# Kernel tuning notes

Hardware: AMD Instinct MI355X
Metric: run time of the kernel (lower is better)

## Reference

```python
import jax, jax.numpy as jnp
import numpy as np

ALPHA = 0.2
NEG = -9e15
EPS = 1e-5


def _gat(h, adj, W, a, out_features):
    # h: [B,N,Fin], adj: [B,N,N], W: [Fin,Fout], a: [2*Fout,1]
    Wh = jnp.matmul(h, W)                      # [B,N,Fout]
    Wh1 = jnp.matmul(Wh, a[:out_features])     # [B,N,1]
    Wh2 = jnp.matmul(Wh, a[out_features:])     # [B,N,1]
    e = Wh1 + jnp.swapaxes(Wh2, 1, 2)          # [B,N,N]
    e = jax.nn.leaky_relu(e, negative_slope=ALPHA)
    scores = jnp.where(adj > 0, e, NEG)
    att = jax.nn.softmax(scores, axis=1)       # NOTE: dim=1 as in source
    return jnp.matmul(att, Wh)                 # [B,N,Fout]


def _layernorm(x, g, b):
    mu = jnp.mean(x, axis=-1, keepdims=True)
    var = jnp.var(x, axis=-1, keepdims=True)
    return (x - mu) * jax.lax.rsqrt(var + EPS) * g + b


def setup_inputs() -> dict:
    key = jax.random.key(0)
    ks = jax.random.split(key, 8)
    B, N, F, H = 2, 4096, 256, 1024
    x = jax.random.normal(ks[0], (B, N, F), dtype=jnp.float32)
    adj = jax.random.randint(ks[1], (B, N, N), 0, 2, dtype=jnp.int32)
    def xavier(k, shape):
        fan_in, fan_out = shape[0], shape[1]
        lim = np.sqrt(6.0 / (fan_in + fan_out))
        return jax.random.uniform(k, shape, jnp.float32, -lim, lim)
    return {
        "x": x,
        "adj": adj,
        "W1": xavier(ks[2], (F, F)),
        "a1": xavier(ks[3], (2 * F, 1)),
        "W2": xavier(ks[4], (F, F)),
        "a2": xavier(ks[5], (2 * F, 1)),
        "w_ff1": xavier(ks[6], (F, H)) ,
        "b_ff1": jnp.zeros((H,), jnp.float32),
        "w_ff2": xavier(ks[7], (H, F)),
        "b_ff2": jnp.zeros((F,), jnp.float32),
        "g_ln1": jnp.ones((F,), jnp.float32),
        "b_ln1": jnp.zeros((F,), jnp.float32),
        "g_ln2": jnp.ones((F,), jnp.float32),
        "b_ln2": jnp.zeros((F,), jnp.float32),
    }


def reference(x, adj, W1, a1, W2, a2, w_ff1, b_ff1, w_ff2, b_ff2,
              g_ln1, b_ln1, g_ln2, b_ln2):
    Fout = W1.shape[1]
    residual = x
    # dropout is a no-op in eval mode
    h = _gat(x, adj, W1, a1, Fout)          # single head -> cat is identity
    h = _gat(h, adj, W2, a2, W2.shape[1])
    h = _layernorm(residual + h, g_ln1, b_ln1)
    residual2 = h
    ff = jnp.matmul(jax.nn.relu(jnp.matmul(h, w_ff1) + b_ff1), w_ff2) + b_ff2
    return _layernorm(residual2 + ff, g_ln2, b_ln2)
```

## Files before the change

kernel.cpp:

```cpp
#include <hip/hip_runtime.h>
#include <math.h>

#define ALPHA 0.2f
#define NEGV  -9e15f
#define EPSV  1e-5f

constexpr int B_ = 2, N_ = 4096, F_ = 256, H_ = 1024;
constexpr int SPLIT_ = 16;
constexpr int SPLITJ_ = 4;

typedef __attribute__((ext_vector_type(4))) float f32x4;
typedef __attribute__((ext_vector_type(8))) short s16x8;

__device__ __forceinline__ unsigned short f2bf(float f) {
    unsigned u = __builtin_bit_cast(unsigned, f);
    u += 0x7fffu + ((u >> 16) & 1u);
    return (unsigned short)(u >> 16);
}

__global__ __launch_bounds__(256) void gemm_bf16_kernel(
    const float* __restrict__ A, const unsigned short* __restrict__ Wt,
    const float* __restrict__ bias, float* __restrict__ C,
    int M, int Nc, int K, int relu)
{
    __shared__ unsigned short As[64 * 72];
    __shared__ unsigned short Bs[64 * 72];
    const int t = threadIdx.x;
    const int w = t >> 6, l = t & 63;
    const int quad = l >> 4, l15 = l & 15;
    const int iw = (w & 1) * 32, fw = (w >> 1) * 32;
    const int row0 = blockIdx.y * 64, col0 = blockIdx.x * 64;

    const int sr = t >> 2;
    const int sk = (t & 3) * 16;

    f32x4 acc[2][2];
    #pragma unroll
    for (int a = 0; a < 2; ++a)
        #pragma unroll
        for (int c = 0; c < 2; ++c) acc[a][c] = (f32x4)(0.f);

    for (int k0 = 0; k0 < K; k0 += 64) {
        {
            const float* ap = &A[(size_t)(row0 + sr) * K + k0 + sk];
            #pragma unroll
            for (int u4 = 0; u4 < 4; ++u4) {
                const float4 v = *(const float4*)&ap[u4 * 4];
                ushort4 o;
                o.x = f2bf(v.x); o.y = f2bf(v.y); o.z = f2bf(v.z); o.w = f2bf(v.w);
                *(ushort4*)&As[sr * 72 + sk + u4 * 4] = o;
            }
        }
        {
            const unsigned short* bp = &Wt[(size_t)(col0 + sr) * K + k0 + sk];
            *(s16x8*)&Bs[sr * 72 + sk]     = *(const s16x8*)bp;
            *(s16x8*)&Bs[sr * 72 + sk + 8] = *(const s16x8*)(bp + 8);
        }
        __syncthreads();
        #pragma unroll
        for (int ks = 0; ks < 64; ks += 32) {
            s16x8 af[2], bf[2];
            #pragma unroll
            for (int it = 0; it < 2; ++it)
                af[it] = *(const s16x8*)&As[(iw + it * 16 + l15) * 72 + ks + quad * 8];
            #pragma unroll
            for (int ft = 0; ft < 2; ++ft)
                bf[ft] = *(const s16x8*)&Bs[(fw + ft * 16 + l15) * 72 + ks + quad * 8];
            #pragma unroll
            for (int it = 0; it < 2; ++it)
                #pragma unroll
                for (int ft = 0; ft < 2; ++ft)
                    acc[it][ft] = __builtin_amdgcn_mfma_f32_16x16x32_bf16(
                        af[it], bf[ft], acc[it][ft], 0, 0, 0);
        }
        __syncthreads();
    }

    #pragma unroll
    for (int ft = 0; ft < 2; ++ft) {
        const int col = col0 + fw + ft * 16 + l15;
        const float bv = bias ? bias[col] : 0.f;
        #pragma unroll
        for (int it = 0; it < 2; ++it) {
            #pragma unroll
            for (int rr = 0; rr < 4; ++rr) {
                const int row = row0 + iw + it * 16 + quad * 4 + rr;
                float v = acc[it][ft][rr] + bv;
                if (relu) v = fmaxf(v, 0.f);
                C[(size_t)row * Nc + col] = v;
            }
        }
    }
}

__global__ __launch_bounds__(256) void wh12_kernel(
    const float* __restrict__ Wh, const float* __restrict__ a,
    float* __restrict__ Wh1, float* __restrict__ Wh2)
{
    const int wid = threadIdx.x >> 6, lane = threadIdx.x & 63;
    const int row = blockIdx.x * 4 + wid;
    const float4 w  = *(const float4*)&Wh[(size_t)row * F_ + lane * 4];
    const float4 u1 = *(const float4*)&a[lane * 4];
    const float4 u2 = *(const float4*)&a[F_ + lane * 4];
    float s1 = w.x * u1.x + w.y * u1.y + w.z * u1.z + w.w * u1.w;
    float s2 = w.x * u2.x + w.y * u2.y + w.z * u2.z + w.w * u2.w;
    #pragma unroll
    for (int off = 32; off > 0; off >>= 1) {
        s1 += __shfl_down(s1, off);
        s2 += __shfl_down(s2, off);
    }
    if (lane == 0) { Wh1[row] = s1; Wh2[row] = s2; }
}

__global__ __launch_bounds__(256) void maskpack_kernel(
    const int* __restrict__ adj, unsigned long long* __restrict__ mask)
{
    const int t = threadIdx.x;
    const int w = t >> 6, l = t & 63;
    const int wid = blockIdx.x * 4 + w;
    const int nw = gridDim.x * 4;
    const int nchunks = (B_ * N_ * N_) / 256;
    for (int c = wid; c < nchunks; c += nw) {
        const size_t base = (size_t)c * 256;
        #pragma unroll
        for (int r = 0; r < 4; ++r) {
            const int v = adj[base + r * 64 + l];
            const unsigned long long bm = __ballot(v > 0);
            if (l == 0) mask[base / 64 + r] = bm;
        }
    }
}

__global__ __launch_bounds__(256) void colstats3_kernel(
    const unsigned long long* __restrict__ mask,
    const float* __restrict__ Wh1, const float* __restrict__ Wh2,
    float* __restrict__ pM, float* __restrict__ pS)
{
    const int t = threadIdx.x;
    const int j = blockIdx.x * 256 + t;
    const int sp = blockIdx.y;
    const int b = blockIdx.z;
    const int i0 = sp * (N_ / SPLIT_);
    const int w = t >> 6;
    const int jbit = t & 63;
    const float w2 = Wh2[b * N_ + j];
    const unsigned long long* __restrict__ mbase =
        mask + ((size_t)b * N_ + i0) * (N_ / 64) + blockIdx.x * 4 + w;
    const float* __restrict__ w1p = Wh1 + b * N_ + i0;

    float m = -3.4e38f, s = 0.f;
    for (int c = 0; c < N_ / SPLIT_; c += 8) {
        float x[8];
        #pragma unroll
        for (int u = 0; u < 8; ++u) {
            const unsigned long long mw = mbase[(size_t)(c + u) * (N_ / 64)];
            const float e0 = w1p[c + u] + w2;
            const float e = fmaxf(e0, ALPHA * e0);
            x[u] = ((mw >> jbit) & 1ull) ? e : NEGV;
        }
        float cm = fmaxf(fmaxf(fmaxf(x[0], x[1]), fmaxf(x[2], x[3])),
                         fmaxf(fmaxf(x[4], x[5]), fmaxf(x[6], x[7])));
        const float nm = fmaxf(m, cm);
        float cs = 0.f;
        #pragma unroll
        for (int u = 0; u < 8; ++u) cs += __expf(x[u] - nm);
        s = s * __expf(m - nm) + cs;
        m = nm;
    }
    pM[((size_t)b * SPLIT_ + sp) * N_ + j] = m;
    pS[((size_t)b * SPLIT_ + sp) * N_ + j] = s;
}

__global__ __launch_bounds__(256) void colfin_kernel(
    const float* __restrict__ pM, const float* __restrict__ pS,
    float* __restrict__ Mcol, float* __restrict__ Sinv)
{
    const int j = blockIdx.x * 256 + threadIdx.x;
    const int b = blockIdx.y;
    float m = -3.4e38f;
    #pragma unroll
    for (int s = 0; s < SPLIT_; ++s)
        m = fmaxf(m, pM[((size_t)b * SPLIT_ + s) * N_ + j]);
    float sum = 0.f;
    #pragma unroll
    for (int s = 0; s < SPLIT_; ++s)
        sum += pS[((size_t)b * SPLIT_ + s) * N_ + j] *
               __expf(pM[((size_t)b * SPLIT_ + s) * N_ + j] - m);
    Mcol[b * N_ + j] = m;
    Sinv[b * N_ + j] = 1.0f / sum;
}

__global__ __launch_bounds__(256) void transp_kernel(
    const float* __restrict__ src, unsigned short* __restrict__ dst, int R, int Cc)
{
    __shared__ float T[64][65];
    const int t = threadIdx.x;
    const int r0 = blockIdx.x * 64, c0 = blockIdx.y * 64;
    const size_t boff = (size_t)blockIdx.z * R * Cc;
    #pragma unroll
    for (int s = 0; s < 4; ++s) {
        const int rr = s * 16 + (t >> 4);
        const int cq = t & 15;
        const float4 v = *(const float4*)&src[boff + (size_t)(r0 + rr) * Cc + c0 + cq * 4];
        T[rr][cq * 4 + 0] = v.x; T[rr][cq * 4 + 1] = v.y;
        T[rr][cq * 4 + 2] = v.z; T[rr][cq * 4 + 3] = v.w;
    }
    __syncthreads();
    #pragma unroll
    for (int s = 0; s < 4; ++s) {
        const int cr = s * 16 + (t >> 4);
        const int rq = t & 15;
        ushort4 o;
        o.x = f2bf(T[rq * 4 + 0][cr]);
        o.y = f2bf(T[rq * 4 + 1][cr]);
        o.z = f2bf(T[rq * 4 + 2][cr]);
        o.w = f2bf(T[rq * 4 + 3][cr]);
        *(ushort4*)&dst[boff + (size_t)(c0 + cr) * R + r0 + rq * 4] = o;
    }
}

__global__ __launch_bounds__(256) void att_mfma2_kernel(
    const unsigned short* __restrict__ mask16, const unsigned short* __restrict__ Wht,
    const float* __restrict__ Wh1, const float* __restrict__ Wh2,
    const float* __restrict__ Mcol, const float* __restrict__ Sinv,
    float* __restrict__ part)
{
    __shared__ unsigned short Bs[256 * 72];
    __shared__ unsigned short Ps[64 * 72];

    const int t = threadIdx.x;
    const int w = t >> 6, l = t & 63;
    const int quad = l >> 4, l15 = l & 15;
    const int b = blockIdx.z;
    const int i0 = blockIdx.x * 64;
    const int sp = blockIdx.y;
    const int jbase = sp * (N_ / SPLITJ_);

    const int pi = t >> 2;
    const int pj4 = t & 3;
    const float w1i = Wh1[b * N_ + i0 + pi];
    const unsigned short* __restrict__ mrow =
        mask16 + ((size_t)b * N_ + i0 + pi) * (N_ / 16);

    f32x4 acc[4][4];
    #pragma unroll
    for (int it = 0; it < 4; ++it)
        #pragma unroll
        for (int ft = 0; ft < 4; ++ft) acc[it][ft] = (f32x4)(0.f);

    const unsigned short* __restrict__ WhtB = Wht + (size_t)b * F_ * N_;
    const float* __restrict__ w2B = Wh2 + b * N_;
    const float* __restrict__ mB  = Mcol + b * N_;
    const float* __restrict__ sB  = Sinv + b * N_;

    for (int itr = 0; itr < (N_ / SPLITJ_) / 64; ++itr) {
        const int jb = jbase + itr * 64;
        #pragma unroll
        for (int s = 0; s < 8; ++s) {
            const int idx = t + s * 256;
            const int f = idx >> 3, prt = idx & 7;
            *(s16x8*)&Bs[f * 72 + prt * 8] =
                *(const s16x8*)&WhtB[(size_t)f * N_ + jb + prt * 8];
        }
        {
            const unsigned mb = mrow[jb / 16 + pj4];
            #pragma unroll
            for (int u4 = 0; u4 < 4; ++u4) {
                const int jo = pj4 * 16 + u4 * 4;
                const float4 w2v = *(const float4*)&w2B[jb + jo];
                const float4 mv  = *(const float4*)&mB[jb + jo];
                const float4 sv  = *(const float4*)&sB[jb + jo];
                ushort4 o;
                unsigned short* op = &o.x;
                #pragma unroll
                for (int u = 0; u < 4; ++u) {
                    const float xw = w1i + (&w2v.x)[u];
                    const float e = fmaxf(xw, ALPHA * xw);
                    const float x2 = ((mb >> (u4 * 4 + u)) & 1u) ? e : NEGV;
                    op[u] = f2bf(__expf(x2 - (&mv.x)[u]) * (&sv.x)[u]);
                }
                *(ushort4*)&Ps[pi * 72 + jo] = o;
            }
        }
        __syncthreads();
        #pragma unroll
        for (int ks = 0; ks < 64; ks += 32) {
            s16x8 af[4];
            #pragma unroll
            for (int it = 0; it < 4; ++it)
                af[it] = *(const s16x8*)&Ps[(it * 16 + l15) * 72 + ks + quad * 8];
            #pragma unroll
            for (int ft = 0; ft < 4; ++ft) {
                const s16x8 bf =
                    *(const s16x8*)&Bs[(w * 64 + ft * 16 + l15) * 72 + ks + quad * 8];
                #pragma unroll
                for (int it = 0; it < 4; ++it)
                    acc[it][ft] = __builtin_amdgcn_mfma_f32_16x16x32_bf16(
                        af[it], bf, acc[it][ft], 0, 0, 0);
            }
        }
        __syncthreads();
    }

    float* __restrict__ pout = part + ((size_t)sp * B_ + b) * N_ * F_;
    #pragma unroll
    for (int it = 0; it < 4; ++it)
        #pragma unroll
        for (int ft = 0; ft < 4; ++ft) {
            const int col = w * 64 + ft * 16 + l15;
            #pragma unroll
            for (int rr = 0; rr < 4; ++rr) {
                const int row = i0 + it * 16 + quad * 4 + rr;
                pout[(size_t)row * F_ + col] = acc[it][ft][rr];
            }
        }
}

__global__ __launch_bounds__(256) void reduce4_kernel(
    const float* __restrict__ p, float* __restrict__ out)
{
    const size_t i = ((size_t)blockIdx.x * 256 + threadIdx.x) * 4;
    const size_t S = (size_t)B_ * N_ * F_;
    const float4 a = *(const float4*)&p[i];
    const float4 b = *(const float4*)&p[i + S];
    const float4 c = *(const float4*)&p[i + 2 * S];
    const float4 d = *(const float4*)&p[i + 3 * S];
    float4 o;
    o.x = a.x + b.x + c.x + d.x;
    o.y = a.y + b.y + c.y + d.y;
    o.z = a.z + b.z + c.z + d.z;
    o.w = a.w + b.w + c.w + d.w;
    *(float4*)&out[i] = o;
}

__global__ __launch_bounds__(256) void addln_kernel(
    const float* __restrict__ X, const float* __restrict__ Y,
    const float* __restrict__ g, const float* __restrict__ bta,
    float* __restrict__ out)
{
    const int row = blockIdx.x;
    const int t = threadIdx.x;
    const size_t idx = (size_t)row * F_ + t;
    const float v = X[idx] + Y[idx];
    float s1 = v, s2 = v * v;
    #pragma unroll
    for (int off = 32; off > 0; off >>= 1) {
        s1 += __shfl_down(s1, off);
        s2 += __shfl_down(s2, off);
    }
    __shared__ float r1[4], r2[4];
    __shared__ float mu_s, rs_s;
    const int wid = t >> 6, lane = t & 63;
    if (lane == 0) { r1[wid] = s1; r2[wid] = s2; }
    __syncthreads();
    if (t == 0) {
        const float a = r1[0] + r1[1] + r1[2] + r1[3];
        const float q = r2[0] + r2[1] + r2[2] + r2[3];
        const float mu = a * (1.f / F_);
        const float var = q * (1.f / F_) - mu * mu;
        mu_s = mu;
        rs_s = rsqrtf(var + EPSV);
    }
    __syncthreads();
    out[idx] = (v - mu_s) * rs_s * g[t] + bta[t];
}

extern "C" void kernel_launch(void* const* d_in, const int* in_sizes, int n_in,
                              void* d_out, int out_size, void* d_ws, size_t ws_size,
                              hipStream_t stream)
{
    const float* x     = (const float*)d_in[0];
    const int*   adj   = (const int*)d_in[1];
    const float* W1    = (const float*)d_in[2];
    const float* a1    = (const float*)d_in[3];
    const float* W2    = (const float*)d_in[4];
    const float* a2    = (const float*)d_in[5];
    const float* w_ff1 = (const float*)d_in[6];
    const float* b_ff1 = (const float*)d_in[7];
    const float* w_ff2 = (const float*)d_in[8];
    const float* b_ff2 = (const float*)d_in[9];
    const float* g_ln1 = (const float*)d_in[10];
    const float* b_ln1 = (const float*)d_in[11];
    const float* g_ln2 = (const float*)d_in[12];
    const float* b_ln2 = (const float*)d_in[13];
    float* out = (float*)d_out;

    const int Rtot = B_ * N_;
    float* ws = (float*)d_ws;
    float* Wh_buf = ws;
    float* ln1    = ws;
    float* g1out  = ws + 2097152;
    float* part   = ws + 4194304;
    float* mid    = ws + 4194304;
    unsigned short* Wht = (unsigned short*)(ws + 12582912);
    unsigned short* Wt  = (unsigned short*)(ws + 12582912);
    unsigned long long* mask = (unsigned long long*)(ws + 13631488);
    unsigned short* mask16 = (unsigned short*)mask;
    float* Wh1v = ws + 14680064;
    float* Wh2v = Wh1v + 8192;
    float* Mcol = Wh2v + 8192;
    float* Sinv = Mcol + 8192;
    float* pM   = Sinv + 8192;
    float* pS   = pM + (size_t)B_ * SPLIT_ * N_;

    const dim3 statsG(N_ / 256, SPLIT_, B_);
    const dim3 finG(N_ / 256, B_);
    const dim3 attG(N_ / 64, SPLITJ_, B_);
    const dim3 trWhG(N_ / 64, F_ / 64, B_);

    maskpack_kernel<<<2048, 256, 0, stream>>>(adj, mask);

    transp_kernel<<<dim3(4, 4, 1), 256, 0, stream>>>(W1, Wt, 256, 256);
    gemm_bf16_kernel<<<dim3(F_ / 64, Rtot / 64), 256, 0, stream>>>(x, Wt, nullptr, Wh_buf, Rtot, F_, F_, 0);
    wh12_kernel<<<Rtot / 4, 256, 0, stream>>>(Wh_buf, a1, Wh1v, Wh2v);
    colstats3_kernel<<<statsG, 256, 0, stream>>>(mask, Wh1v, Wh2v, pM, pS);
    colfin_kernel<<<finG, 256, 0, stream>>>(pM, pS, Mcol, Sinv);
    transp_kernel<<<trWhG, 256, 0, stream>>>(Wh_buf, Wht, N_, F_);
    att_mfma2_kernel<<<attG, 256, 0, stream>>>(mask16, Wht, Wh1v, Wh2v, Mcol, Sinv, part);
    reduce4_kernel<<<2048, 256, 0, stream>>>(part, g1out);

    transp_kernel<<<dim3(4, 4, 1), 256, 0, stream>>>(W2, Wt, 256, 256);
    gemm_bf16_kernel<<<dim3(F_ / 64, Rtot / 64), 256, 0, stream>>>(g1out, Wt, nullptr, Wh_buf, Rtot, F_, F_, 0);
    wh12_kernel<<<Rtot / 4, 256, 0, stream>>>(Wh_buf, a2, Wh1v, Wh2v);
    colstats3_kernel<<<statsG, 256, 0, stream>>>(mask, Wh1v, Wh2v, pM, pS);
    colfin_kernel<<<finG, 256, 0, stream>>>(pM, pS, Mcol, Sinv);
    transp_kernel<<<trWhG, 256, 0, stream>>>(Wh_buf, Wht, N_, F_);
    att_mfma2_kernel<<<attG, 256, 0, stream>>>(mask16, Wht, Wh1v, Wh2v, Mcol, Sinv, part);
    reduce4_kernel<<<2048, 256, 0, stream>>>(part, g1out);

    addln_kernel<<<Rtot, 256, 0, stream>>>(x, g1out, g_ln1, b_ln1, ln1);

    transp_kernel<<<dim3(4, 16, 1), 256, 0, stream>>>(w_ff1, Wt, 256, 1024);
    gemm_bf16_kernel<<<dim3(H_ / 64, Rtot / 64), 256, 0, stream>>>(ln1, Wt, b_ff1, mid, Rtot, H_, F_, 1);
    transp_kernel<<<dim3(16, 4, 1), 256, 0, stream>>>(w_ff2, Wt, 1024, 256);
    gemm_bf16_kernel<<<dim3(F_ / 64, Rtot / 64), 256, 0, stream>>>(mid, Wt, b_ff2, out, Rtot, F_, H_, 0);

    addln_kernel<<<Rtot, 256, 0, stream>>>(ln1, out, g_ln2, b_ln2, out);
}
```

Before: 464.6 us.

## Fuse mask packing into column stats, GEMM transposed output, and log-sum-exp softmax

Several changes at once. The adjacency bitmask is now packed inside the first column-stats pass, which drops the separate maskpack pass over the int32 adj. The Wh GEMM writes a transposed bf16 copy of its output directly, removing the standalone transpose kernels. The softmax normalizer is folded into one log-sum-exp value, so the attention kernel loads one fewer vector, caches Wh2 and Mo in shared memory, and prefetches the next Wht tile into registers. The FFN intermediate is also stored in bf16 to halve its traffic, at some precision cost and with a larger workspace footprint.

```diff
diff --git a/kernel.cpp b/kernel.cpp
--- a/kernel.cpp
+++ b/kernel.cpp
@@ -18,10 +18,11 @@
     return (unsigned short)(u >> 16);
 }
 
-__global__ __launch_bounds__(256) void gemm_bf16_kernel(
-    const float* __restrict__ A, const unsigned short* __restrict__ Wt,
-    const float* __restrict__ bias, float* __restrict__ C,
-    int M, int Nc, int K, int relu)
+__global__ __launch_bounds__(256) void gemm2_kernel(
+    const void* __restrict__ Ap, const unsigned short* __restrict__ Wt,
+    const float* __restrict__ bias, void* __restrict__ Cp,
+    unsigned short* __restrict__ Tout,
+    int M, int Nc, int K, int relu, int a_bf16, int c_bf16)
 {
     __shared__ unsigned short As[64 * 72];
     __shared__ unsigned short Bs[64 * 72];
@@ -41,8 +42,13 @@
         for (int c = 0; c < 2; ++c) acc[a][c] = (f32x4)(0.f);
 
     for (int k0 = 0; k0 < K; k0 += 64) {
-        {
-            const float* ap = &A[(size_t)(row0 + sr) * K + k0 + sk];
+        if (a_bf16) {
+            const unsigned short* ap =
+                (const unsigned short*)Ap + (size_t)(row0 + sr) * K + k0 + sk;
+            *(s16x8*)&As[sr * 72 + sk]     = *(const s16x8*)ap;
+            *(s16x8*)&As[sr * 72 + sk + 8] = *(const s16x8*)(ap + 8);
+        } else {
+            const float* ap = (const float*)Ap + (size_t)(row0 + sr) * K + k0 + sk;
             #pragma unroll
             for (int u4 = 0; u4 < 4; ++u4) {
                 const float4 v = *(const float4*)&ap[u4 * 4];
@@ -82,12 +88,33 @@
         const float bv = bias ? bias[col] : 0.f;
         #pragma unroll
         for (int it = 0; it < 2; ++it) {
-            #pragma unroll
-            for (int rr = 0; rr < 4; ++rr) {
-                const int row = row0 + iw + it * 16 + quad * 4 + rr;
-                float v = acc[it][ft][rr] + bv;
-                if (relu) v = fmaxf(v, 0.f);
-                C[(size_t)row * Nc + col] = v;
+            float v0 = acc[it][ft][0] + bv, v1 = acc[it][ft][1] + bv;
+            float v2 = acc[it][ft][2] + bv, v3 = acc[it][ft][3] + bv;
+            if (relu) {
+                v0 = fmaxf(v0, 0.f); v1 = fmaxf(v1, 0.f);
+                v2 = fmaxf(v2, 0.f); v3 = fmaxf(v3, 0.f);
+            }
+            const int rbase = row0 + iw + it * 16 + quad * 4;
+            if (c_bf16) {
+                unsigned short* Cs = (unsigned short*)Cp;
+                Cs[(size_t)(rbase + 0) * Nc + col] = f2bf(v0);
+                Cs[(size_t)(rbase + 1) * Nc + col] = f2bf(v1);
+                Cs[(size_t)(rbase + 2) * Nc + col] = f2bf(v2);
+                Cs[(size_t)(rbase + 3) * Nc + col] = f2bf(v3);
+            } else {
+                float* Cf = (float*)Cp;
+                Cf[(size_t)(rbase + 0) * Nc + col] = v0;
+                Cf[(size_t)(rbase + 1) * Nc + col] = v1;
+                Cf[(size_t)(rbase + 2) * Nc + col] = v2;
+                Cf[(size_t)(rbase + 3) * Nc + col] = v3;
+            }
+            if (Tout) {
+                const int bb = row0 >> 12;
+                const int ibase = (row0 & (N_ - 1)) + iw + it * 16 + quad * 4;
+                ushort4 o;
+                o.x = f2bf(acc[it][ft][0]); o.y = f2bf(acc[it][ft][1]);
+                o.z = f2bf(acc[it][ft][2]); o.w = f2bf(acc[it][ft][3]);
+                *(ushort4*)&Tout[((size_t)bb * F_ + col) * N_ + ibase] = o;
             }
         }
     }
@@ -112,23 +139,48 @@
     if (lane == 0) { Wh1[row] = s1; Wh2[row] = s2; }
 }
 
-__global__ __launch_bounds__(256) void maskpack_kernel(
-    const int* __restrict__ adj, unsigned long long* __restrict__ mask)
+__global__ __launch_bounds__(256) void colstats_adj_kernel(
+    const int* __restrict__ adj, unsigned long long* __restrict__ maskOut,
+    const float* __restrict__ Wh1, const float* __restrict__ Wh2,
+    float* __restrict__ pM, float* __restrict__ pS)
 {
     const int t = threadIdx.x;
+    const int j = blockIdx.x * 256 + t;
+    const int sp = blockIdx.y;
+    const int b = blockIdx.z;
+    const int i0 = sp * (N_ / SPLIT_);
     const int w = t >> 6, l = t & 63;
-    const int wid = blockIdx.x * 4 + w;
-    const int nw = gridDim.x * 4;
-    const int nchunks = (B_ * N_ * N_) / 256;
-    for (int c = wid; c < nchunks; c += nw) {
-        const size_t base = (size_t)c * 256;
-        #pragma unroll
-        for (int r = 0; r < 4; ++r) {
-            const int v = adj[base + r * 64 + l];
-            const unsigned long long bm = __ballot(v > 0);
-            if (l == 0) mask[base / 64 + r] = bm;
-        }
-    }
+    const float w2 = Wh2[b * N_ + j];
+    const float* __restrict__ w1p = Wh1 + b * N_ + i0;
+    const int* __restrict__ ap = adj + ((size_t)b * N_ + i0) * N_ + j;
+
+    float m = -3.4e38f, s = 0.f;
+    for (int c = 0; c < N_ / SPLIT_; c += 8) {
+        int v[8];
+        #pragma unroll
+        for (int u = 0; u < 8; ++u) v[u] = ap[(size_t)(c + u) * N_];
+        float x[8];
+        #pragma unroll
+        for (int u = 0; u < 8; ++u) {
+            const bool act = v[u] > 0;
+            const unsigned long long bm = __ballot(act);
+            if (l == 0)
+                maskOut[((size_t)b * N_ + i0 + c + u) * (N_ / 64) + blockIdx.x * 4 + w] = bm;
+            const float e0 = w1p[c + u] + w2;
+            const float e = fmaxf(e0, ALPHA * e0);
+            x[u] = act ? e : NEGV;
+        }
+        const float cm = fmaxf(fmaxf(fmaxf(x[0], x[1]), fmaxf(x[2], x[3])),
+                               fmaxf(fmaxf(x[4], x[5]), fmaxf(x[6], x[7])));
+        const float nm = fmaxf(m, cm);
+        float cs = 0.f;
+        #pragma unroll
+        for (int u = 0; u < 8; ++u) cs += __expf(x[u] - nm);
+        s = s * __expf(m - nm) + cs;
+        m = nm;
+    }
+    pM[((size_t)b * SPLIT_ + sp) * N_ + j] = m;
+    pS[((size_t)b * SPLIT_ + sp) * N_ + j] = s;
 }
 
 __global__ __launch_bounds__(256) void colstats3_kernel(
@@ -158,8 +210,8 @@
             const float e = fmaxf(e0, ALPHA * e0);
             x[u] = ((mw >> jbit) & 1ull) ? e : NEGV;
         }
-        float cm = fmaxf(fmaxf(fmaxf(x[0], x[1]), fmaxf(x[2], x[3])),
-                         fmaxf(fmaxf(x[4], x[5]), fmaxf(x[6], x[7])));
+        const float cm = fmaxf(fmaxf(fmaxf(x[0], x[1]), fmaxf(x[2], x[3])),
+                               fmaxf(fmaxf(x[4], x[5]), fmaxf(x[6], x[7])));
         const float nm = fmaxf(m, cm);
         float cs = 0.f;
         #pragma unroll
@@ -171,9 +223,9 @@
     pS[((size_t)b * SPLIT_ + sp) * N_ + j] = s;
 }
 
-__global__ __launch_bounds__(256) void colfin_kernel(
+__global__ __launch_bounds__(256) void colfin2_kernel(
     const float* __restrict__ pM, const float* __restrict__ pS,
-    float* __restrict__ Mcol, float* __restrict__ Sinv)
+    float* __restrict__ Mo)
 {
     const int j = blockIdx.x * 256 + threadIdx.x;
     const int b = blockIdx.y;
@@ -186,8 +238,7 @@
     for (int s = 0; s < SPLIT_; ++s)
         sum += pS[((size_t)b * SPLIT_ + s) * N_ + j] *
                __expf(pM[((size_t)b * SPLIT_ + s) * N_ + j] - m);
-    Mcol[b * N_ + j] = m;
-    Sinv[b * N_ + j] = 1.0f / sum;
+    Mo[b * N_ + j] = m + logf(sum);
 }
 
 __global__ __launch_bounds__(256) void transp_kernel(
@@ -196,12 +247,11 @@
     __shared__ float T[64][65];
     const int t = threadIdx.x;
     const int r0 = blockIdx.x * 64, c0 = blockIdx.y * 64;
-    const size_t boff = (size_t)blockIdx.z * R * Cc;
     #pragma unroll
     for (int s = 0; s < 4; ++s) {
         const int rr = s * 16 + (t >> 4);
         const int cq = t & 15;
-        const float4 v = *(const float4*)&src[boff + (size_t)(r0 + rr) * Cc + c0 + cq * 4];
+        const float4 v = *(const float4*)&src[(size_t)(r0 + rr) * Cc + c0 + cq * 4];
         T[rr][cq * 4 + 0] = v.x; T[rr][cq * 4 + 1] = v.y;
         T[rr][cq * 4 + 2] = v.z; T[rr][cq * 4 + 3] = v.w;
     }
@@ -215,18 +265,19 @@
         o.y = f2bf(T[rq * 4 + 1][cr]);
         o.z = f2bf(T[rq * 4 + 2][cr]);
         o.w = f2bf(T[rq * 4 + 3][cr]);
-        *(ushort4*)&dst[boff + (size_t)(c0 + cr) * R + r0 + rq * 4] = o;
-    }
-}
-
-__global__ __launch_bounds__(256) void att_mfma2_kernel(
+        *(ushort4*)&dst[(size_t)(c0 + cr) * R + r0 + rq * 4] = o;
+    }
+}
+
+__global__ __launch_bounds__(256) void att_mfma3_kernel(
     const unsigned short* __restrict__ mask16, const unsigned short* __restrict__ Wht,
     const float* __restrict__ Wh1, const float* __restrict__ Wh2,
-    const float* __restrict__ Mcol, const float* __restrict__ Sinv,
-    float* __restrict__ part)
+    const float* __restrict__ Mo, float* __restrict__ part)
 {
     __shared__ unsigned short Bs[256 * 72];
     __shared__ unsigned short Ps[64 * 72];
+    __shared__ float w2s[1024];
+    __shared__ float mos[1024];
 
     const int t = threadIdx.x;
     const int w = t >> 6, l = t & 63;
@@ -241,6 +292,14 @@
     const float w1i = Wh1[b * N_ + i0 + pi];
     const unsigned short* __restrict__ mrow =
         mask16 + ((size_t)b * N_ + i0 + pi) * (N_ / 16);
+    const unsigned short* __restrict__ WhtB = Wht + (size_t)b * F_ * N_;
+
+    {
+        const float4 a = *(const float4*)&Wh2[b * N_ + jbase + t * 4];
+        const float4 c = *(const float4*)&Mo[b * N_ + jbase + t * 4];
+        *(float4*)&w2s[t * 4] = a;
+        *(float4*)&mos[t * 4] = c;
+    }
 
     f32x4 acc[4][4];
     #pragma unroll
@@ -248,28 +307,31 @@
         #pragma unroll
         for (int ft = 0; ft < 4; ++ft) acc[it][ft] = (f32x4)(0.f);
 
-    const unsigned short* __restrict__ WhtB = Wht + (size_t)b * F_ * N_;
-    const float* __restrict__ w2B = Wh2 + b * N_;
-    const float* __restrict__ mB  = Mcol + b * N_;
-    const float* __restrict__ sB  = Sinv + b * N_;
-
-    for (int itr = 0; itr < (N_ / SPLITJ_) / 64; ++itr) {
+    const int f0s = t >> 3;
+    const int prt = (t & 7) * 8;
+    s16x8 breg[8];
+    {
+        const int jb = jbase;
+        #pragma unroll
+        for (int s = 0; s < 8; ++s)
+            breg[s] = *(const s16x8*)&WhtB[(size_t)(f0s + s * 32) * N_ + jb + prt];
+    }
+    unsigned short mb_cur = mrow[jbase / 16 + pj4];
+    __syncthreads();
+
+    constexpr int NITER = (N_ / SPLITJ_) / 64;
+    for (int itr = 0; itr < NITER; ++itr) {
         const int jb = jbase + itr * 64;
         #pragma unroll
-        for (int s = 0; s < 8; ++s) {
-            const int idx = t + s * 256;
-            const int f = idx >> 3, prt = idx & 7;
-            *(s16x8*)&Bs[f * 72 + prt * 8] =
-                *(const s16x8*)&WhtB[(size_t)f * N_ + jb + prt * 8];
-        }
+        for (int s = 0; s < 8; ++s)
+            *(s16x8*)&Bs[(f0s + s * 32) * 72 + prt] = breg[s];
         {
-            const unsigned mb = mrow[jb / 16 + pj4];
+            const unsigned mb = mb_cur;
+            const int jl = itr * 64 + pj4 * 16;
             #pragma unroll
             for (int u4 = 0; u4 < 4; ++u4) {
-                const int jo = pj4 * 16 + u4 * 4;
-                const float4 w2v = *(const float4*)&w2B[jb + jo];
-                const float4 mv  = *(const float4*)&mB[jb + jo];
-                const float4 sv  = *(const float4*)&sB[jb + jo];
+                const float4 w2v = *(const float4*)&w2s[jl + u4 * 4];
+                const float4 mov = *(const float4*)&mos[jl + u4 * 4];
                 ushort4 o;
                 unsigned short* op = &o.x;
                 #pragma unroll
@@ -277,12 +339,19 @@
                     const float xw = w1i + (&w2v.x)[u];
                     const float e = fmaxf(xw, ALPHA * xw);
                     const float x2 = ((mb >> (u4 * 4 + u)) & 1u) ? e : NEGV;
-                    op[u] = f2bf(__expf(x2 - (&mv.x)[u]) * (&sv.x)[u]);
+                    op[u] = f2bf(__expf(x2 - (&mov.x)[u]));
                 }
-                *(ushort4*)&Ps[pi * 72 + jo] = o;
+                *(ushort4*)&Ps[pi * 72 + pj4 * 16 + u4 * 4] = o;
             }
         }
         __syncthreads();
+        if (itr + 1 < NITER) {
+            const int jn = jb + 64;
+            #pragma unroll
+            for (int s = 0; s < 8; ++s)
+                breg[s] = *(const s16x8*)&WhtB[(size_t)(f0s + s * 32) * N_ + jn + prt];
+            mb_cur = mrow[jn / 16 + pj4];
+        }
         #pragma unroll
         for (int ks = 0; ks < 64; ks += 32) {
             s16x8 af[4];
@@ -388,52 +457,50 @@
     const int Rtot = B_ * N_;
     float* ws = (float*)d_ws;
     float* Wh_buf = ws;
-    float* ln1    = ws;
     float* g1out  = ws + 2097152;
-    float* part   = ws + 4194304;
-    float* mid    = ws + 4194304;
-    unsigned short* Wht = (unsigned short*)(ws + 12582912);
-    unsigned short* Wt  = (unsigned short*)(ws + 12582912);
-    unsigned long long* mask = (unsigned long long*)(ws + 13631488);
+    float* ln1    = ws + 4194304;
+    float* part   = ws + 6291456;
+    unsigned short* mid_us = (unsigned short*)(ws + 14680064);
+    unsigned short* Wht    = (unsigned short*)(ws + 18874368);
+    unsigned long long* mask = (unsigned long long*)(ws + 19922944);
     unsigned short* mask16 = (unsigned short*)mask;
-    float* Wh1v = ws + 14680064;
+    float* Wh1v = ws + 20971520;
     float* Wh2v = Wh1v + 8192;
-    float* Mcol = Wh2v + 8192;
-    float* Sinv = Mcol + 8192;
-    float* pM   = Sinv + 8192;
+    float* Mo   = Wh2v + 8192;
+    float* pM   = Mo + 8192;
     float* pS   = pM + (size_t)B_ * SPLIT_ * N_;
+    unsigned short* Wt = (unsigned short*)(ws + 21299200);
 
     const dim3 statsG(N_ / 256, SPLIT_, B_);
     const dim3 finG(N_ / 256, B_);
     const dim3 attG(N_ / 64, SPLITJ_, B_);
-    const dim3 trWhG(N_ / 64, F_ / 64, B_);
-
-    maskpack_kernel<<<2048, 256, 0, stream>>>(adj, mask);
-
-    transp_kernel<<<dim3(4, 4, 1), 256, 0, stream>>>(W1, Wt, 256, 256);
-    gemm_bf16_kernel<<<dim3(F_ / 64, Rtot / 64), 256, 0, stream>>>(x, Wt, nullptr, Wh_buf, Rtot, F_, F_, 0);
+
+    transp_kernel<<<dim3(4, 4), 256, 0, stream>>>(W1, Wt, 256, 256);
+    gemm2_kernel<<<dim3(F_ / 64, Rtot / 64), 256, 0, stream>>>(
+        x, Wt, nullptr, Wh_buf, Wht, Rtot, F_, F_, 0, 0, 0);
     wh12_kernel<<<Rtot / 4, 256, 0, stream>>>(Wh_buf, a1, Wh1v, Wh2v);
-    colstats3_kernel<<<statsG, 256, 0, stream>>>(mask, Wh1v, Wh2v, pM, pS);
-    colfin_kernel<<<finG, 256, 0, stream>>>(pM, pS, Mcol, Sinv);
-    transp_kernel<<<trWhG, 256, 0, stream>>>(Wh_buf, Wht, N_, F_);
-    att_mfma2_kernel<<<attG, 256, 0, stream>>>(mask16, Wht, Wh1v, Wh2v, Mcol, Sinv, part);
+    colstats_adj_kernel<<<statsG, 256, 0, stream>>>(adj, mask, Wh1v, Wh2v, pM, pS);
+    colfin2_kernel<<<finG, 256, 0, stream>>>(pM, pS, Mo);
+    att_mfma3_kernel<<<attG, 256, 0, stream>>>(mask16, Wht, Wh1v, Wh2v, Mo, part);
     reduce4_kernel<<<2048, 256, 0, stream>>>(part, g1out);
 
-    transp_kernel<<<dim3(4, 4, 1), 256, 0, stream>>>(W2, Wt, 256, 256);
-    gemm_bf16_kernel<<<dim3(F_ / 64, Rtot / 64), 256, 0, stream>>>(g1out, Wt, nullptr, Wh_buf, Rtot, F_, F_, 0);
+    transp_kernel<<<dim3(4, 4), 256, 0, stream>>>(W2, Wt, 256, 256);
+    gemm2_kernel<<<dim3(F_ / 64, Rtot / 64), 256, 0, stream>>>(
+        g1out, Wt, nullptr, Wh_buf, Wht, Rtot, F_, F_, 0, 0, 0);
     wh12_kernel<<<Rtot / 4, 256, 0, stream>>>(Wh_buf, a2, Wh1v, Wh2v);
     colstats3_kernel<<<statsG, 256, 0, stream>>>(mask, Wh1v, Wh2v, pM, pS);
-    colfin_kernel<<<finG, 256, 0, stream>>>(pM, pS, Mcol, Sinv);
-    transp_kernel<<<trWhG, 256, 0, stream>>>(Wh_buf, Wht, N_, F_);
-    att_mfma2_kernel<<<attG, 256, 0, stream>>>(mask16, Wht, Wh1v, Wh2v, Mcol, Sinv, part);
+    colfin2_kernel<<<finG, 256, 0, stream>>>(pM, pS, Mo);
+    att_mfma3_kernel<<<attG, 256, 0, stream>>>(mask16, Wht, Wh1v, Wh2v, Mo, part);
     reduce4_kernel<<<2048, 256, 0, stream>>>(part, g1out);
 
     addln_kernel<<<Rtot, 256, 0, stream>>>(x, g1out, g_ln1, b_ln1, ln1);
 
-    transp_kernel<<<dim3(4, 16, 1), 256, 0, stream>>>(w_ff1, Wt, 256, 1024);
-    gemm_bf16_kernel<<<dim3(H_ / 64, Rtot / 64), 256, 0, stream>>>(ln1, Wt, b_ff1, mid, Rtot, H_, F_, 1);
-    transp_kernel<<<dim3(16, 4, 1), 256, 0, stream>>>(w_ff2, Wt, 1024, 256);
-    gemm_bf16_kernel<<<dim3(F_ / 64, Rtot / 64), 256, 0, stream>>>(mid, Wt, b_ff2, out, Rtot, F_, H_, 0);
+    transp_kernel<<<dim3(4, 16), 256, 0, stream>>>(w_ff1, Wt, 256, 1024);
+    gemm2_kernel<<<dim3(H_ / 64, Rtot / 64), 256, 0, stream>>>(
+        ln1, Wt, b_ff1, mid_us, nullptr, Rtot, H_, F_, 1, 0, 1);
+    transp_kernel<<<dim3(16, 4), 256, 0, stream>>>(w_ff2, Wt, 1024, 256);
+    gemm2_kernel<<<dim3(F_ / 64, Rtot / 64), 256, 0, stream>>>(
+        mid_us, Wt, b_ff2, out, nullptr, Rtot, F_, H_, 0, 1, 0);
 
     addln_kernel<<<Rtot, 256, 0, stream>>>(ln1, out, g_ln2, b_ln2, out);
 }
```

Measured after the change: 424.0 us. -8.7%, faster.
